# Kernel tuning notes

Hardware: AMD Instinct MI355X
Metric: run time of the kernel (lower is better)

Reference implementation:

```python
import jax, jax.numpy as jnp
import numpy as np

THETA = 0.5  # forward default arg
ALPHA = 0.2  # LeakyReLU negative slope
NEG_INF = -9e15


def setup_inputs() -> dict:
    key = jax.random.key(0)
    k1, k2, k3, k4, k5 = jax.random.split(key, 5)
    N, F_IN, F_OUT = 8192, 256, 256
    h = jax.random.normal(k1, (N, F_IN), dtype=jnp.float32)
    adj = jax.random.randint(k2, (N, N), 0, 2, dtype=jnp.int32)
    cv_values = jax.random.uniform(k3, (N,), dtype=jnp.float32)
    # xavier_uniform with gain=1.414
    g = 1.414
    bw = g * np.sqrt(6.0 / (F_IN + F_OUT))
    W = jax.random.uniform(k4, (F_IN, F_OUT), dtype=jnp.float32, minval=-bw, maxval=bw)
    ba = g * np.sqrt(6.0 / (2 * F_OUT + 1))
    a = jax.random.uniform(k5, (2 * F_OUT, 1), dtype=jnp.float32, minval=-ba, maxval=ba)
    return {"h": h, "adj": adj, "cv_values": cv_values, "W": W, "a": a}


def reference(h, adj, cv_values, W, a):
    # Wh: [N, F_out]
    Wh = h @ W
    F_out = Wh.shape[1]
    a1 = a[:F_out, 0]   # [F_out]
    a2 = a[F_out:, 0]   # [F_out]
    # e_ij = LeakyReLU([Wh_i ; Wh_j] . a) = LeakyReLU(Wh_i.a1 + Wh_j.a2)
    f1 = Wh @ a1        # [N]
    f2 = Wh @ a2        # [N]
    e = jax.nn.leaky_relu(f1[:, None] + f2[None, :], negative_slope=ALPHA)
    # CV bias: theta * cv_i broadcast across row i
    e = e + THETA * cv_values[:, None]
    att = jnp.where(adj > 0, e, jnp.float32(NEG_INF))
    att = jax.nn.softmax(att, axis=1)
    # dropout is identity in eval mode (training=False)
    h_prime = att @ Wh  # [N, F_out]
    return jax.nn.elu(h_prime)  # concat=True branch
```

## Files before the change

### kernel.cpp

```cpp
#include <hip/hip_runtime.h>
#include <cstdint>
#include <cstddef>

typedef _Float16 half8 __attribute__((ext_vector_type(8)));
typedef _Float16 half4 __attribute__((ext_vector_type(4)));
typedef float f32x4 __attribute__((ext_vector_type(4)));
typedef int iv4 __attribute__((ext_vector_type(4)));

#define GAT_N 8192
#define GAT_F 256
#define GAT_NQ 8
#define GAT_ALPHA 0.2f
#define GAT_LOG2E 1.4426950408889634f

__device__ inline unsigned enc_f32(float x) {
    unsigned b = __float_as_uint(x);
    return (b & 0x80000000u) ? ~b : (b | 0x80000000u);
}
__device__ inline float dec_f32(unsigned u) {
    unsigned b = (u & 0x80000000u) ? (u ^ 0x80000000u) : ~u;
    return __uint_as_float(b);
}

__device__ inline unsigned pack8(iv4 v0, iv4 v1) {
    return (unsigned)(v0[0] > 0)        | ((unsigned)(v0[1] > 0) << 1)
         | ((unsigned)(v0[2] > 0) << 2) | ((unsigned)(v0[3] > 0) << 3)
         | ((unsigned)(v1[0] > 0) << 4) | ((unsigned)(v1[1] > 0) << 5)
         | ((unsigned)(v1[2] > 0) << 6) | ((unsigned)(v1[3] > 0) << 7);
}


__global__ __launch_bounds__(256) void gat_k0b_convert(
    const float* __restrict__ W, _Float16* __restrict__ WT,
    unsigned* __restrict__ f2mxEnc)
{
    const int g = blockIdx.x * 256 + threadIdx.x;
    if (g == 0) *f2mxEnc = 0u;
    const int k = g >> 8, n = g & 255;
    WT[n * GAT_F + k] = (_Float16)W[g];
}

__global__ __launch_bounds__(256, 2) void gat_k1_gemm(
    const float* __restrict__ h, const _Float16* __restrict__ WT,
    const float* __restrict__ a, _Float16* __restrict__ whT2,
    float* __restrict__ f1L, float* __restrict__ f2L,
    unsigned* __restrict__ f2mxEnc)
{
    __shared__ float sP1[4][16], sP2[4][16];
    const int wv = threadIdx.x >> 6;
    const int lane = threadIdx.x & 63;
    const int l15 = lane & 15;
    const int quad = lane >> 4;
    const int r0 = blockIdx.x * 16;

    f32x4 acc[4];
    #pragma unroll
    for (int t = 0; t < 4; ++t) { f32x4 z = {0.f,0.f,0.f,0.f}; acc[t] = z; }

    #pragma unroll
    for (int k0 = 0; k0 < GAT_F; k0 += 32) {
        const float* ap = h + (size_t)(r0 + l15) * GAT_F + k0 + quad * 8;
        const float4 a0 = *reinterpret_cast<const float4*>(ap);
        const float4 a1 = *reinterpret_cast<const float4*>(ap + 4);
        half8 af;
        af[0] = (_Float16)a0.x; af[1] = (_Float16)a0.y;
        af[2] = (_Float16)a0.z; af[3] = (_Float16)a0.w;
        af[4] = (_Float16)a1.x; af[5] = (_Float16)a1.y;
        af[6] = (_Float16)a1.z; af[7] = (_Float16)a1.w;
        #pragma unroll
        for (int t = 0; t < 4; ++t) {
            half8 bf = *reinterpret_cast<const half8*>(
                WT + (size_t)(wv * 64 + t * 16 + l15) * GAT_F + k0 + quad * 8);
            acc[t] = __builtin_amdgcn_mfma_f32_16x16x32_f16(af, bf, acc[t], 0, 0, 0);
        }
    }

    float p1[4] = {0.f,0.f,0.f,0.f}, p2[4] = {0.f,0.f,0.f,0.f};
    #pragma unroll
    for (int t = 0; t < 4; ++t) {
        float a1c = a[wv * 64 + t * 16 + l15];
        float a2c = a[GAT_F + wv * 64 + t * 16 + l15];
        #pragma unroll
        for (int r = 0; r < 4; ++r) {
            p1[r] = fmaf(acc[t][r], a1c, p1[r]);
            p2[r] = fmaf(acc[t][r], a2c, p2[r]);
        }
    }
    #pragma unroll
    for (int off = 1; off < 16; off <<= 1) {
        #pragma unroll
        for (int r = 0; r < 4; ++r) {
            p1[r] += __shfl_xor(p1[r], off);
            p2[r] += __shfl_xor(p2[r], off);
        }
    }
    if (l15 == 0) {
        #pragma unroll
        for (int r = 0; r < 4; ++r) {
            sP1[wv][quad * 4 + r] = p1[r];
            sP2[wv][quad * 4 + r] = p2[r];
        }
    }
    __syncthreads();
    if (threadIdx.x < 16) {
        const int row = threadIdx.x;
        const float s1 = (sP1[0][row] + sP1[1][row] + sP1[2][row] + sP1[3][row]) * GAT_LOG2E;
        const float s2 = (sP2[0][row] + sP2[1][row] + sP2[2][row] + sP2[3][row]) * GAT_LOG2E;
        f1L[r0 + row] = s1;
        f2L[r0 + row] = s2;
        float mx = s2;
        #pragma unroll
        for (int off = 1; off < 16; off <<= 1) mx = fmaxf(mx, __shfl_xor(mx, off));
        if (row == 0) atomicMax(f2mxEnc, enc_f32(mx));
    }

    const size_t tbase = (size_t)(r0 >> 6) * 16384
                       + (((r0 & 63) >> 3) + (quad >> 1)) * 2048
                       + (quad & 1) * 4;
    #pragma unroll
    for (int t = 0; t < 4; ++t) {
        const int c = wv * 64 + t * 16 + l15;
        half4 hv;
        #pragma unroll
        for (int r = 0; r < 4; ++r) hv[r] = (_Float16)acc[t][r];
        *reinterpret_cast<half4*>(whT2 + tbase + c * 8) = hv;
    }
}

__global__ __launch_bounds__(256, 4) void gat_k3_attn(
    const int* __restrict__ adj, const float* __restrict__ f1L,
    const float* __restrict__ f2L, const unsigned* __restrict__ f2mxEnc,
    const _Float16* __restrict__ whT2,
    _Float16* __restrict__ Ph,
    float* __restrict__ L)
{
    __shared__ __align__(16) _Float16 sB[2][8192];
    __shared__ __align__(16) float sF2[1024];

    const int bx = blockIdx.x;
    const int q  = bx & 7;
    const int rb = bx >> 3;
    const int wv = threadIdx.x >> 6;
    const int lane = threadIdx.x & 63;
    const int l15 = lane & 15;
    const int quad = lane >> 4;

    const int kq = q * 1024;
    const int r0 = rb * 64 + wv * 16;
    const int rA = r0 + l15;

    const float fmxL = dec_f32(*f2mxEnc);
    const float f1A = f1L[rA];
    const float sAv = f1A + fmxL;
    const float CA = fmaxf(sAv, GAT_ALPHA * sAv);
    const float uA = f1A - CA, vA = GAT_ALPHA * f1A - CA;

    {
        const float4 v = *reinterpret_cast<const float4*>(f2L + kq + threadIdx.x * 4);
        *reinterpret_cast<float4*>(&sF2[threadIdx.x * 4]) = v;
    }

    f32x4 acc[16];
    #pragma unroll
    for (int t = 0; t < 16; ++t) { f32x4 z = {0.f,0.f,0.f,0.f}; acc[t] = z; }
    float d0 = 0.f;

    const int* aprA = adj + (size_t)rA * GAT_N + kq + quad * 8;

    iv4 xA0, xA1;
    #define ADJLOAD(s)                                                         \
        {                                                                      \
            const int* pa = aprA + (s) * 32;                                   \
            xA0 = *reinterpret_cast<const iv4*>(pa);                           \
            xA1 = *reinterpret_cast<const iv4*>(pa + 4);                       \
        }
    #define ADJPACK(m) { m = pack8(xA0, xA1); }

    const _Float16* tile0 = whT2 + (size_t)(q * 32) * 8192
                          + wv * 2048 + (size_t)lane * 8;
    #define STAGE(buf, step)                                                   \
        {                                                                      \
            _Pragma("unroll")                                                  \
            for (int i = 0; i < 4; ++i) {                                      \
                const _Float16* gp = tile0 + (size_t)(step) * 8192 + i * 512;  \
                _Float16* lp = &sB[buf][wv * 2048 + i * 512];                  \
                __builtin_amdgcn_global_load_lds(                              \
                    (const __attribute__((address_space(1))) void*)gp,         \
                    (__attribute__((address_space(3))) void*)lp, 16, 0, 0);    \
            }                                                                  \
        }

    unsigned cmA, nmA;
    ADJLOAD(0)
    STAGE(0, 0)
    ADJPACK(cmA)
    __syncthreads();

    const _Float16* const sflat = &sB[0][0];

    for (int step = 0; step < 32; ++step) {
        const int cur = step & 1;
        if (step < 31) {
            ADJLOAD(step + 1)
            STAGE(1 - cur, step + 1)
        }

        const float* fp = &sF2[step * 32 + quad * 8];
        const float4 cfa = *reinterpret_cast<const float4*>(fp);
        const float4 cfb = *reinterpret_cast<const float4*>(fp + 4);
        const float f2v[8] = {cfa.x, cfa.y, cfa.z, cfa.w,
                              cfb.x, cfb.y, cfb.z, cfb.w};
        float af2[8];
        #pragma unroll
        for (int j = 0; j < 8; ++j) af2[j] = GAT_ALPHA * f2v[j];

        half8 pA;
        #pragma unroll
        for (int j = 0; j < 8; ++j) {
            float pa = __builtin_amdgcn_exp2f(fmaxf(uA + f2v[j], vA + af2[j]));
            pa = (cmA & (1u << j)) ? pa : 0.f;
            d0 += pa;
            pA[j] = (_Float16)pa;
        }

        const _Float16* bk = sflat + cur * 8192 + quad * 2048 + l15 * 8;
        __builtin_amdgcn_s_setprio(1);
        #pragma unroll
        for (int t = 0; t < 16; ++t) {
            half8 bf = *reinterpret_cast<const half8*>(bk + t * 128);
            acc[t] = __builtin_amdgcn_mfma_f32_16x16x32_f16(pA, bf, acc[t], 0, 0, 0);
        }
        __builtin_amdgcn_s_setprio(0);

        if (step < 31) {
            ADJPACK(nmA)
            cmA = nmA;
            __syncthreads();
        }
    }
    #undef STAGE
    #undef ADJLOAD
    #undef ADJPACK

    d0 += __shfl_xor(d0, 16); d0 += __shfl_xor(d0, 32);
    if (lane < 16) L[q * GAT_N + rA] = d0;

    const int wid = rb * 4 + wv;
    _Float16* Pq = Ph + ((size_t)q * 512 + wid) * 4096;
    #pragma unroll
    for (int t = 0; t < 16; ++t) {
        half4 hv;
        #pragma unroll
        for (int r = 0; r < 4; ++r) hv[r] = (_Float16)acc[t][r];
        __builtin_nontemporal_store(hv,
            reinterpret_cast<half4*>(Pq + (size_t)((t * 64 + lane) * 4)));
    }
}

__global__ __launch_bounds__(256) void gat_k4_final(
    const _Float16* __restrict__ Ph, const float* __restrict__ L,
    float* __restrict__ out)
{
    const int tid = threadIdx.x;
    const int wid = blockIdx.x >> 2;
    __shared__ float s_rl[16];
    if (tid < 16) {
        const int row = wid * 16 + tid;
        float s = 0.f;
        #pragma unroll
        for (int q = 0; q < GAT_NQ; ++q) s += L[q * GAT_N + row];
        s_rl[tid] = 1.0f / fmaxf(s, 1e-30f);
    }
    __syncthreads();

    const int idx = blockIdx.x * 256 + tid;
    const int rem = idx & 1023;
    const int lane = rem & 63;
    const int t = rem >> 6;
    const int l15 = lane & 15, quad = lane >> 4;
    const int lrow0 = quad * 4;
    const int col = t * 16 + l15;

    float accv[4] = {0.f, 0.f, 0.f, 0.f};
    #pragma unroll
    for (int q = 0; q < GAT_NQ; ++q) {
        half4 v = *reinterpret_cast<const half4*>(
            Ph + ((size_t)q * 512 + wid) * 4096 + (size_t)rem * 4);
        #pragma unroll
        for (int r = 0; r < 4; ++r) accv[r] += (float)v[r];
    }
    #pragma unroll
    for (int r = 0; r < 4; ++r) {
        const float v = accv[r] * s_rl[lrow0 + r];
        const float o = v > 0.f ? v : expm1f(v);
        out[(size_t)(wid * 16 + lrow0 + r) * GAT_F + col] = o;
    }
}

extern "C" void kernel_launch(void* const* d_in, const int* in_sizes, int n_in,
                              void* d_out, int out_size, void* d_ws, size_t ws_size,
                              hipStream_t stream)
{
    const float* h   = (const float*)d_in[0];
    const int*   adj = (const int*)d_in[1];
    const float* W   = (const float*)d_in[3];
    const float* a   = (const float*)d_in[4];
    float* out = (float*)d_out;
    char* ws = (char*)d_ws;

    const size_t SLAB = (size_t)GAT_N * GAT_F * 2;

    size_t off = 0;
    _Float16* whT2 = (_Float16*)(ws + off); off += SLAB;
    _Float16* Ph  = (_Float16*)(ws + off); off += GAT_NQ * SLAB;
    _Float16* WT  = (_Float16*)(ws + off); off += (size_t)GAT_F * GAT_F * 2;
    float* f1L = (float*)(ws + off); off += GAT_N * 4;
    float* f2L = (float*)(ws + off); off += GAT_N * 4;
    float* L   = (float*)(ws + off); off += GAT_NQ * GAT_N * 4;
    unsigned* f2mxEnc = (unsigned*)(ws + off); off += 256;

    gat_k0b_convert<<<256, 256, 0, stream>>>(W, WT, f2mxEnc);
    gat_k1_gemm<<<512, 256, 0, stream>>>(h, WT, a, whT2, f1L, f2L, f2mxEnc);
    gat_k3_attn<<<1024, 256, 0, stream>>>(adj, f1L, f2L, f2mxEnc, whT2, Ph, L);
    gat_k4_final<<<2048, 256, 0, stream>>>(Ph, L, out);
}
```

Measured before the change: 433.8 us.

## Stream adjacency tiles through LDS with async loads two steps ahead

Adjacency row chunks were loaded into registers one step ahead. They are now fetched straight into a double-buffered LDS array with global_load_lds, issued two steps ahead. Manual vmcnt waits and sched_barriers control when the mask is read and packed. The goal is to hide adj memory latency, which dominates this 256MB int32 stream. The extra shared memory lowers the occupancy hint from 4 to 3 blocks per CU, and the hand-counted waitcnts are fragile.

After: 459.9 us. 6.0% more time.

```diff
diff --git a/kernel.cpp b/kernel.cpp
--- a/kernel.cpp
+++ b/kernel.cpp
@@ -127,7 +127,7 @@
     }
 }
 
-__global__ __launch_bounds__(256, 4) void gat_k3_attn(
+__global__ __launch_bounds__(256, 3) void gat_k3_attn(
     const int* __restrict__ adj, const float* __restrict__ f1L,
     const float* __restrict__ f2L, const unsigned* __restrict__ f2mxEnc,
     const _Float16* __restrict__ whT2,
@@ -136,6 +136,7 @@
 {
     __shared__ __align__(16) _Float16 sB[2][8192];
     __shared__ __align__(16) float sF2[1024];
+    __shared__ __align__(16) int sAdj[2][4][512];
 
     const int bx = blockIdx.x;
     const int q  = bx & 7;
@@ -165,16 +166,27 @@
     for (int t = 0; t < 16; ++t) { f32x4 z = {0.f,0.f,0.f,0.f}; acc[t] = z; }
     float d0 = 0.f;
 
-    const int* aprA = adj + (size_t)rA * GAT_N + kq + quad * 8;
-
-    iv4 xA0, xA1;
-    #define ADJLOAD(s)                                                         \
+    const int* adjB0 = adj + (size_t)r0 * GAT_N + kq;
+    #define ADJGL(slot, s)                                                     \
         {                                                                      \
-            const int* pa = aprA + (s) * 32;                                   \
-            xA0 = *reinterpret_cast<const iv4*>(pa);                           \
-            xA1 = *reinterpret_cast<const iv4*>(pa + 4);                       \
-        }
-    #define ADJPACK(m) { m = pack8(xA0, xA1); }
+            _Pragma("unroll")                                                  \
+            for (int k = 0; k < 2; ++k) {                                      \
+                const int* gp = adjB0 + (size_t)(lane & 15) * GAT_N            \
+                              + (s) * 32 + (k * 4 + (lane >> 4)) * 4;          \
+                int* lp = &sAdj[slot][wv][k * 256];                            \
+                __builtin_amdgcn_global_load_lds(                              \
+                    (const __attribute__((address_space(1))) void*)gp,         \
+                    (__attribute__((address_space(3))) void*)lp, 16, 0, 0);    \
+            }                                                                  \
+        }
+    #define ADJREAD_PACK(slot, m)                                              \
+        {                                                                      \
+            iv4 a0 = *reinterpret_cast<const iv4*>(                            \
+                &sAdj[slot][wv][(quad * 2) * 64 + l15 * 4]);                   \
+            iv4 a1 = *reinterpret_cast<const iv4*>(                            \
+                &sAdj[slot][wv][(quad * 2 + 1) * 64 + l15 * 4]);               \
+            m = pack8(a0, a1);                                                 \
+        }
 
     const _Float16* tile0 = whT2 + (size_t)(q * 32) * 8192
                           + wv * 2048 + (size_t)lane * 8;
@@ -190,20 +202,25 @@
             }                                                                  \
         }
 
-    unsigned cmA, nmA;
-    ADJLOAD(0)
+    unsigned cmA;
     STAGE(0, 0)
-    ADJPACK(cmA)
+    ADJGL(1, 1)
+    {
+        const int* pa = adj + (size_t)rA * GAT_N + kq + quad * 8;
+        iv4 x0 = *reinterpret_cast<const iv4*>(pa);
+        iv4 x1 = *reinterpret_cast<const iv4*>(pa + 4);
+        cmA = pack8(x0, x1);
+    }
     __syncthreads();
 
     const _Float16* const sflat = &sB[0][0];
 
     for (int step = 0; step < 32; ++step) {
         const int cur = step & 1;
-        if (step < 31) {
-            ADJLOAD(step + 1)
-            STAGE(1 - cur, step + 1)
-        }
+        if (step < 31) STAGE(1 - cur, step + 1)
+        __builtin_amdgcn_sched_barrier(0);
+        if (step < 30) ADJGL(step & 1, step + 2)
+        __builtin_amdgcn_sched_barrier(0);
 
         const float* fp = &sF2[step * 32 + quad * 8];
         const float4 cfa = *reinterpret_cast<const float4*>(fp);
@@ -233,14 +250,19 @@
         __builtin_amdgcn_s_setprio(0);
 
         if (step < 31) {
-            ADJPACK(nmA)
-            cmA = nmA;
-            __syncthreads();
+            if (step < 30) { asm volatile("s_waitcnt vmcnt(6)" ::: "memory"); }
+            else           { asm volatile("s_waitcnt vmcnt(4)" ::: "memory"); }
+            __builtin_amdgcn_sched_barrier(0);
+            ADJREAD_PACK((step + 1) & 1, cmA)
+            if (step < 30) { asm volatile("s_waitcnt vmcnt(2)" ::: "memory"); }
+            else           { asm volatile("s_waitcnt vmcnt(0)" ::: "memory"); }
+            __builtin_amdgcn_sched_barrier(0);
+            __builtin_amdgcn_s_barrier();
         }
     }
     #undef STAGE
-    #undef ADJLOAD
-    #undef ADJPACK
+    #undef ADJGL
+    #undef ADJREAD_PACK
 
     d0 += __shfl_xor(d0, 16); d0 += __shfl_xor(d0, 32);
     if (lane < 16) L[q * GAT_N + rA] = d0;
```
